# Optimization experiments

Hardware: AMD Instinct MI355X
Metric: run time of the kernel (lower is better)

Reference implementation:

```python
import jax, jax.numpy as jnp
import numpy as np

HEADS = 6
G = 4  # redundant group repeat factor in the original module
EPS = 1e-5


def _dw_bn(x, w, gamma, beta, mean, var):
    # depthwise 3x3 conv (stride 1, pad 1, no bias) + BatchNorm (eval mode)
    C = x.shape[1]
    y = jax.lax.conv_general_dilated(
        x, w, window_strides=(1, 1), padding=[(1, 1), (1, 1)],
        dimension_numbers=('NCHW', 'OIHW', 'NCHW'), feature_group_count=C)
    inv = gamma / jnp.sqrt(var + EPS)
    return y * inv[None, :, None, None] + (beta - mean * inv)[None, :, None, None]


def setup_inputs() -> dict:
    key = jax.random.key(0)
    ks = jax.random.split(key, 20)
    B, Cin, Cout, H, W = 8, 192, 192, 28, 28
    inp = {
        'x': jax.random.normal(ks[0], (B, H * W, Cin), jnp.float32),
        'h': H, 'w': W,
    }
    s = 0.1
    for i, p in enumerate(['q', 'k', 'v']):
        inp[f'dw{p}_w'] = jax.random.normal(ks[1 + i], (Cin, 1, 3, 3), jnp.float32) * s
        bk = jax.random.split(ks[4 + i], 4)
        inp[f'bn{p}_g'] = 1.0 + 0.1 * jax.random.normal(bk[0], (Cin,), jnp.float32)
        inp[f'bn{p}_b'] = 0.1 * jax.random.normal(bk[1], (Cin,), jnp.float32)
        inp[f'bn{p}_m'] = 0.1 * jax.random.normal(bk[2], (Cin,), jnp.float32)
        inp[f'bn{p}_v'] = jax.random.uniform(bk[3], (Cin,), jnp.float32, 0.5, 1.5)
        inp[f'p{p}_w'] = jax.random.normal(ks[7 + i], (Cout, Cin), jnp.float32) * (Cin ** -0.5)
        inp[f'p{p}_b'] = 0.01 * jax.random.normal(ks[10 + i], (Cout,), jnp.float32)
    inp['po_w'] = jax.random.normal(ks[13], (Cout, Cout), jnp.float32) * (Cout ** -0.5)
    inp['po_b'] = 0.01 * jax.random.normal(ks[14], (Cout,), jnp.float32)
    return inp


def reference(x, h, w,
              dwq_w, bnq_g, bnq_b, bnq_m, bnq_v, pq_w, pq_b,
              dwk_w, bnk_g, bnk_b, bnk_m, bnk_v, pk_w, pk_b,
              dwv_w, bnv_g, bnv_b, bnv_m, bnv_v, pv_w, pv_b,
              po_w, po_b):
    B, N, Cin = x.shape
    Cout = pq_w.shape[0]
    ch = Cout // HEADS  # per-head channel dim
    x4 = jnp.transpose(x, (0, 2, 1)).reshape(B, Cin, h, w)

    q = _dw_bn(x4, dwq_w, bnq_g, bnq_b, bnq_m, bnq_v)
    k = _dw_bn(x4, dwk_w, bnk_g, bnk_b, bnk_m, bnk_v)
    v = _dw_bn(x4, dwv_w, bnv_g, bnv_b, bnv_m, bnv_v)

    # 1x1 conv projections
    q = jnp.einsum('oc,bcij->boij', pq_w, q) + pq_b[None, :, None, None]
    k = jnp.einsum('oc,bcij->boij', pk_w, k) + pk_b[None, :, None, None]
    v = jnp.einsum('oc,bcij->boij', pv_w, v) + pv_b[None, :, None, None]

    # split heads: channels are (head, ch) ordered -> (B, heads, ch, h, w)
    qh = q.reshape(B, HEADS, ch, h, w)
    kh = k.reshape(B, HEADS, ch, h, w)
    vh = v.reshape(B, HEADS, ch, h, w)

    scale = Cout ** -0.5  # NOTE: original scales by dim_out**-0.5, not head_dim
    score = jnp.einsum('bhcij,bhckl->bhijkl', qh, kh) * scale
    attn = jax.nn.softmax(score.reshape(B, HEADS, h, w, h * w), axis=-1)
    attn = attn.reshape(B, HEADS, h, w, h, w)

    out = jnp.einsum('bhijkl,bhckl->bhcij', attn, vh)  # (B, heads, ch, h, w)
    # original output channel order is (ch, heads) via 'b c h g i j -> b (c h) g i j'
    out = jnp.transpose(out, (0, 2, 1, 3, 4))  # (B, ch, heads, h, w)
    out = jnp.broadcast_to(out[:, :, :, None], (B, ch, HEADS, G, h, w))
    out = out.reshape(B, ch * HEADS, G, h, w)

    y = jnp.einsum('oc,bcgij->bogij', po_w, out) + po_b[None, :, None, None, None]
    return y
```

## Files before the change

kernel.cpp:

```cpp
#include <hip/hip_runtime.h>
#include <math.h>

namespace {
constexpr int kB = 8;
constexpr int kC = 192;
constexpr int kH = 28;
constexpr int kW = 28;
constexpr int kN = 784;
constexpr int kHEADS = 6;
constexpr int kG = 4;
constexpr float kEPS = 1e-5f;
constexpr float kSCALE = 0.07216878364870322f;
constexpr int kNP = 800;
constexpr int kXP = 832;

constexpr int kDWB = kB * 196;
constexpr int kWCV = 192;
constexpr int kKVP = 32;
constexpr int kXAP = 192;
}

typedef __attribute__((ext_vector_type(8))) short bf16x8;
typedef __attribute__((ext_vector_type(4))) float f32x4;

static __device__ __forceinline__ unsigned short f2bf(float f) {
    union { float f; unsigned int u; } v; v.f = f;
    unsigned int r = v.u + 0x7fffu + ((v.u >> 16) & 1u);
    return (unsigned short)(r >> 16);
}

__global__ __launch_bounds__(192) void dwprep_kernel(
    const float* __restrict__ x,
    const float* __restrict__ wq, const float* __restrict__ gq,
    const float* __restrict__ bq, const float* __restrict__ mq,
    const float* __restrict__ vq,
    const float* __restrict__ wk, const float* __restrict__ gk,
    const float* __restrict__ bk, const float* __restrict__ mk,
    const float* __restrict__ vk,
    const float* __restrict__ wv, const float* __restrict__ gv,
    const float* __restrict__ bv, const float* __restrict__ mv,
    const float* __restrict__ vv,
    const float* __restrict__ pqw, const float* __restrict__ pkw,
    const float* __restrict__ pvw, const float* __restrict__ pow_,
    unsigned short* __restrict__ xq, unsigned short* __restrict__ xk,
    unsigned short* __restrict__ xv,
    unsigned short* __restrict__ Wq, unsigned short* __restrict__ Wk,
    unsigned short* __restrict__ Wv, unsigned short* __restrict__ Wo,
    unsigned short* __restrict__ Kb, unsigned short* __restrict__ Vb)
{
    const int bx = blockIdx.x;
    const int t = threadIdx.x;

    if (bx < kDWB) {
        const int c = t;
        const int b = bx / 196;
        const int p0 = (bx % 196) * 4;

        float wwq[9], wwk[9], wwv[9];
#pragma unroll
        for (int i = 0; i < 9; ++i) {
            wwq[i] = wq[c * 9 + i];
            wwk[i] = wk[c * 9 + i];
            wwv[i] = wv[c * 9 + i];
        }
        const float invq = gq[c] * rsqrtf(vq[c] + kEPS);
        const float addq = bq[c] - mq[c] * invq;
        const float invk = gk[c] * rsqrtf(vk[c] + kEPS);
        const float addk = bk[c] - mk[c] * invk;
        const float invv = gv[c] * rsqrtf(vv[c] + kEPS);
        const float addv = bv[c] - mv[c] * invv;

        const float* xb = x + (size_t)b * kN * kC + c;
#pragma unroll
        for (int p = 0; p < 4; ++p) {
            const int n = p0 + p;
            const int i = n / kW;
            const int j = n % kW;
            float aq = 0.f, ak = 0.f, av = 0.f;
#pragma unroll
            for (int di = -1; di <= 1; ++di) {
                const int ii = i + di;
                if (ii < 0 || ii >= kH) continue;
#pragma unroll
                for (int dj = -1; dj <= 1; ++dj) {
                    const int jj = j + dj;
                    if (jj < 0 || jj >= kW) continue;
                    const float xvl = xb[(size_t)(ii * kW + jj) * kC];
                    const int tap = (di + 1) * 3 + (dj + 1);
                    aq += xvl * wwq[tap];
                    ak += xvl * wwk[tap];
                    av += xvl * wwv[tap];
                }
            }
            const size_t o = ((size_t)b * kXP + n) * kC + c;
            xq[o] = f2bf(aq * invq + addq);
            xk[o] = f2bf(ak * invk + addk);
            xv[o] = f2bf(av * invv + addv);
        }
    } else if (bx < kDWB + kWCV) {
        const int qidx = (bx - kDWB) * 192 + t;
        const int e0 = qidx * 4;
        const int mat = e0 / (kC * kC);
        const int r = e0 % (kC * kC);
        if (mat < 3) {
            const float* src = (mat == 0) ? pqw : (mat == 1) ? pkw : pvw;
            unsigned short* dst = (mat == 0) ? Wq : (mat == 1) ? Wk : Wv;
            const f32x4 v = *(const f32x4*)&src[r];
            ushort4 p;
            p.x = f2bf(v[0]); p.y = f2bf(v[1]); p.z = f2bf(v[2]); p.w = f2bf(v[3]);
            *(ushort4*)&dst[r] = p;
        } else {
            const int o = r / kC, c0 = r % kC;
            ushort4 p;
            unsigned short* pp = &p.x;
#pragma unroll
            for (int e = 0; e < 4; ++e) {
                const int c = c0 + e;
                pp[e] = f2bf(pow_[o * kC + (c & 31) * kHEADS + (c >> 5)]);
            }
            *(ushort4*)&Wo[o * kC + c0] = p;
        }
    } else if (bx < kDWB + kWCV + kKVP) {
        const int idx8 = (bx - kDWB - kWCV) * 192 + t;
        const ushort4 z = {0, 0, 0, 0};
        if (idx8 < 3072) {
            const int bh = idx8 / 64, k = idx8 % 64;
            unsigned short* p = Kb + (size_t)bh * kNP * 32 + kN * 32 + k * 8;
            *(ushort4*)p = z; *(ushort4*)(p + 4) = z;
        } else {
            const int c2 = idx8 - 3072;
            const int bh = c2 / 64, rem = c2 % 64;
            const int ch = rem >> 1, half = rem & 1;
            unsigned short* p = Vb + ((size_t)bh * 32 + ch) * kNP + kN + half * 8;
            *(ushort4*)p = z; *(ushort4*)(p + 4) = z;
        }
    } else {
        const int c = (bx - kDWB - kWCV - kKVP) * 192 + t;
        const int arr = c / 9216;
        const int r = c % 9216;
        const int b = r / 1152, rem = r % 1152;
        const int row = kN + rem / 24;
        const int col8 = (rem % 24) * 8;
        const size_t XSZ = (size_t)kB * kXP * kC;
        unsigned short* p = xq + (size_t)arr * XSZ + ((size_t)b * kXP + row) * kC + col8;
        const ushort4 z = {0, 0, 0, 0};
        *(ushort4*)p = z; *(ushort4*)(p + 4) = z;
    }
}

__global__ __launch_bounds__(256) void proj_kernel(
    const unsigned short* __restrict__ Xq, const unsigned short* __restrict__ Xk,
    const unsigned short* __restrict__ Xv,
    const unsigned short* __restrict__ Wq, const unsigned short* __restrict__ Wk,
    const unsigned short* __restrict__ Wv,
    const float* __restrict__ bq, const float* __restrict__ bk,
    const float* __restrict__ bv,
    unsigned short* __restrict__ Qb, unsigned short* __restrict__ Kb,
    unsigned short* __restrict__ Vb)
{
    const int br = blockIdx.z % 3;
    const int b  = blockIdx.z / 3;
    const unsigned short* X = (br == 0) ? Xq : (br == 1) ? Xk : Xv;
    const unsigned short* W = (br == 0) ? Wq : (br == 1) ? Wk : Wv;
    const float* bias       = (br == 0) ? bq : (br == 1) ? bk : bv;

    const int n0 = blockIdx.x * 64, o0 = blockIdx.y * 64;
    const int t = threadIdx.x, l = t & 63, w = t >> 6;
    const int q16 = l & 15, u = l >> 4;
    const int ob = o0 + (w >> 1) * 32;
    const int nb = n0 + (w & 1) * 32;

    f32x4 a00 = {0,0,0,0}, a01 = {0,0,0,0}, a10 = {0,0,0,0}, a11 = {0,0,0,0};
    const unsigned short* Wr0 = W + (size_t)(ob + q16) * kC + u * 8;
    const unsigned short* Wr1 = W + (size_t)(ob + 16 + q16) * kC + u * 8;
    const unsigned short* Xr0 = X + ((size_t)b * kXP + nb + q16) * kC + u * 8;
    const unsigned short* Xr1 = X + ((size_t)b * kXP + nb + 16 + q16) * kC + u * 8;
#pragma unroll
    for (int kk = 0; kk < 6; ++kk) {
        const bf16x8 wa0 = *(const bf16x8*)(Wr0 + kk * 32);
        const bf16x8 wa1 = *(const bf16x8*)(Wr1 + kk * 32);
        const bf16x8 xa0 = *(const bf16x8*)(Xr0 + kk * 32);
        const bf16x8 xa1 = *(const bf16x8*)(Xr1 + kk * 32);
        a00 = __builtin_amdgcn_mfma_f32_16x16x32_bf16(wa0, xa0, a00, 0, 0, 0);
        a01 = __builtin_amdgcn_mfma_f32_16x16x32_bf16(wa0, xa1, a01, 0, 0, 0);
        a10 = __builtin_amdgcn_mfma_f32_16x16x32_bf16(wa1, xa0, a10, 0, 0, 0);
        a11 = __builtin_amdgcn_mfma_f32_16x16x32_bf16(wa1, xa1, a11, 0, 0, 0);
    }

    const float sc = (br == 0) ? kSCALE : 1.0f;
#pragma unroll
    for (int ot = 0; ot < 2; ++ot) {
        const int obase = ob + ot * 16;
        const int hh = obase >> 5;
        const int chb = (obase & 31) + 4 * u;
        const f32x4 bi = *(const f32x4*)&bias[obase + 4 * u];
#pragma unroll
        for (int nt = 0; nt < 2; ++nt) {
            const f32x4 A = (ot == 0) ? (nt == 0 ? a00 : a01)
                                      : (nt == 0 ? a10 : a11);
            const int n = nb + nt * 16 + q16;
            if (n >= kNP) continue;
            if (br < 2) {
                ushort4 p;
                p.x = f2bf((A[0] + bi[0]) * sc);
                p.y = f2bf((A[1] + bi[1]) * sc);
                p.z = f2bf((A[2] + bi[2]) * sc);
                p.w = f2bf((A[3] + bi[3]) * sc);
                unsigned short* dst = ((br == 0) ? Qb : Kb) +
                    ((size_t)(b * kHEADS + hh) * kNP + n) * 32 + chb;
                *(ushort4*)dst = p;
            } else {
                unsigned short* dst = Vb +
                    ((size_t)(b * kHEADS + hh) * 32 + chb) * kNP + n;
                dst[0 * kNP] = f2bf(A[0] + bi[0]);
                dst[1 * kNP] = f2bf(A[1] + bi[1]);
                dst[2 * kNP] = f2bf(A[2] + bi[2]);
                dst[3 * kNP] = f2bf(A[3] + bi[3]);
            }
        }
    }
}

__global__ __launch_bounds__(256) void attn_kernel(
    const unsigned short* __restrict__ Qbf, const unsigned short* __restrict__ Kbf,
    const unsigned short* __restrict__ Vbf, unsigned short* __restrict__ AO)
{
    const int wid = blockIdx.x * 4 + (threadIdx.x >> 6);
    const int l = threadIdx.x & 63;
    const int qt = wid % 49;
    const int h  = (wid / 49) % kHEADS;
    const int b  = wid / (49 * kHEADS);
    const int i0 = qt * 16;
    const int q16 = l & 15;
    const int u = l >> 4;

    const unsigned short* Qp = Qbf + ((size_t)(b * kHEADS + h) * kNP + i0) * 32;
    const unsigned short* Kp = Kbf + (size_t)(b * kHEADS + h) * kNP * 32;
    const unsigned short* Vr0 = Vbf + ((size_t)(b * kHEADS + h) * 32 + q16) * kNP;
    const unsigned short* Vr1 = Vr0 + (size_t)16 * kNP;

    const bf16x8 qa = *(const bf16x8*)(Qp + q16 * 32 + u * 8);

    f32x4 oa0 = {0.f, 0.f, 0.f, 0.f};
    f32x4 oa1 = {0.f, 0.f, 0.f, 0.f};
    float m = -1e30f, lsum = 0.f;

    for (int tile = 0; tile < 25; ++tile) {
        const int t0 = tile * 32;
        const bf16x8 ka0 = *(const bf16x8*)(Kp + (size_t)(t0 + q16) * 32 + u * 8);
        const bf16x8 ka1 = *(const bf16x8*)(Kp + (size_t)(t0 + 16 + q16) * 32 + u * 8);
        f32x4 d0 = {0.f, 0.f, 0.f, 0.f};
        f32x4 d1 = {0.f, 0.f, 0.f, 0.f};
        d0 = __builtin_amdgcn_mfma_f32_16x16x32_bf16(ka0, qa, d0, 0, 0, 0);
        d1 = __builtin_amdgcn_mfma_f32_16x16x32_bf16(ka1, qa, d1, 0, 0, 0);
        if (t0 + 16 >= kN) {
            d1[0] = -1e30f; d1[1] = -1e30f; d1[2] = -1e30f; d1[3] = -1e30f;
        }
        float tm = fmaxf(fmaxf(fmaxf(d0[0], d0[1]), fmaxf(d0[2], d0[3])),
                         fmaxf(fmaxf(d1[0], d1[1]), fmaxf(d1[2], d1[3])));
        tm = fmaxf(tm, __shfl_xor(tm, 16));
        tm = fmaxf(tm, __shfl_xor(tm, 32));
        if (!__all(tm <= m + 8.0f)) {
            const float newm = fmaxf(m, tm);
            const float alpha = __expf(m - newm);
            m = newm;
            lsum *= alpha;
            const float al0 = __shfl(alpha, u * 4 + 0);
            const float al1 = __shfl(alpha, u * 4 + 1);
            const float al2 = __shfl(alpha, u * 4 + 2);
            const float al3 = __shfl(alpha, u * 4 + 3);
            oa0[0] *= al0; oa0[1] *= al1; oa0[2] *= al2; oa0[3] *= al3;
            oa1[0] *= al0; oa1[1] *= al1; oa1[2] *= al2; oa1[3] *= al3;
        }
        const float e0 = __expf(d0[0] - m), e1 = __expf(d0[1] - m);
        const float e2 = __expf(d0[2] - m), e3 = __expf(d0[3] - m);
        const float e4 = __expf(d1[0] - m), e5 = __expf(d1[1] - m);
        const float e6 = __expf(d1[2] - m), e7 = __expf(d1[3] - m);
        lsum += (((e0 + e1) + (e2 + e3)) + ((e4 + e5) + (e6 + e7)));
        union { unsigned int w[4]; bf16x8 v; } pa;
        asm("v_cvt_pk_bf16_f32 %0, %1, %2" : "=v"(pa.w[0]) : "v"(e0), "v"(e1));
        asm("v_cvt_pk_bf16_f32 %0, %1, %2" : "=v"(pa.w[1]) : "v"(e2), "v"(e3));
        asm("v_cvt_pk_bf16_f32 %0, %1, %2" : "=v"(pa.w[2]) : "v"(e4), "v"(e5));
        asm("v_cvt_pk_bf16_f32 %0, %1, %2" : "=v"(pa.w[3]) : "v"(e6), "v"(e7));
        union { ushort4 hlf[2]; bf16x8 v; } v0, v1;
        v0.hlf[0] = *(const ushort4*)(Vr0 + t0 + 4 * u);
        v0.hlf[1] = *(const ushort4*)(Vr0 + t0 + 16 + 4 * u);
        v1.hlf[0] = *(const ushort4*)(Vr1 + t0 + 4 * u);
        v1.hlf[1] = *(const ushort4*)(Vr1 + t0 + 16 + 4 * u);
        oa0 = __builtin_amdgcn_mfma_f32_16x16x32_bf16(pa.v, v0.v, oa0, 0, 0, 0);
        oa1 = __builtin_amdgcn_mfma_f32_16x16x32_bf16(pa.v, v1.v, oa1, 0, 0, 0);
    }
    lsum += __shfl_xor(lsum, 16);
    lsum += __shfl_xor(lsum, 32);
    const float rinv = 1.0f / lsum;
    const float r0 = __shfl(rinv, u * 4 + 0);
    const float r1 = __shfl(rinv, u * 4 + 1);
    const float r2 = __shfl(rinv, u * 4 + 2);
    const float r3 = __shfl(rinv, u * 4 + 3);
    unsigned short* aw = AO + ((size_t)b * kXP + i0 + 4 * u) * kC + h * 32 + q16;
    aw[0 * kC + 0]  = f2bf(oa0[0] * r0);
    aw[1 * kC + 0]  = f2bf(oa0[1] * r1);
    aw[2 * kC + 0]  = f2bf(oa0[2] * r2);
    aw[3 * kC + 0]  = f2bf(oa0[3] * r3);
    aw[0 * kC + 16] = f2bf(oa1[0] * r0);
    aw[1 * kC + 16] = f2bf(oa1[1] * r1);
    aw[2 * kC + 16] = f2bf(oa1[2] * r2);
    aw[3 * kC + 16] = f2bf(oa1[3] * r3);
}

__global__ __launch_bounds__(256) void outproj_kernel(
    const unsigned short* __restrict__ AO, const unsigned short* __restrict__ Wo,
    const float* __restrict__ pob, float* __restrict__ Y)
{
    __shared__ float outs[64][68];

    const int b = blockIdx.z;
    const int n0 = blockIdx.x * 64, o0 = blockIdx.y * 64;
    const int t = threadIdx.x, l = t & 63, w = t >> 6;
    const int q16 = l & 15, u = l >> 4;
    const int ob = o0 + w * 16;

    f32x4 c0 = {0,0,0,0}, c1 = {0,0,0,0}, c2 = {0,0,0,0}, c3 = {0,0,0,0};
    const unsigned short* Wr = Wo + (size_t)(ob + q16) * kC + u * 8;
    const unsigned short* Ar = AO + ((size_t)b * kXP + n0 + q16) * kC + u * 8;
#pragma unroll
    for (int kk = 0; kk < 6; ++kk) {
        const bf16x8 a = *(const bf16x8*)(Wr + kk * 32);
        const bf16x8 x0 = *(const bf16x8*)(Ar + (size_t)0 * 16 * kC + kk * 32);
        const bf16x8 x1 = *(const bf16x8*)(Ar + (size_t)1 * 16 * kC + kk * 32);
        const bf16x8 x2 = *(const bf16x8*)(Ar + (size_t)2 * 16 * kC + kk * 32);
        const bf16x8 x3 = *(const bf16x8*)(Ar + (size_t)3 * 16 * kC + kk * 32);
        c0 = __builtin_amdgcn_mfma_f32_16x16x32_bf16(a, x0, c0, 0, 0, 0);
        c1 = __builtin_amdgcn_mfma_f32_16x16x32_bf16(a, x1, c1, 0, 0, 0);
        c2 = __builtin_amdgcn_mfma_f32_16x16x32_bf16(a, x2, c2, 0, 0, 0);
        c3 = __builtin_amdgcn_mfma_f32_16x16x32_bf16(a, x3, c3, 0, 0, 0);
    }
    const f32x4 bi = *(const f32x4*)&pob[ob + 4 * u];
#pragma unroll
    for (int nt = 0; nt < 4; ++nt) {
        const f32x4 A = (nt == 0) ? c0 : (nt == 1) ? c1 : (nt == 2) ? c2 : c3;
#pragma unroll
        for (int r = 0; r < 4; ++r)
            outs[w * 16 + 4 * u + r][nt * 16 + q16] = A[r] + bi[r];
    }
    __syncthreads();

    const int ol = t >> 2;
    const int nq = (t & 3) * 16;
    const int nbase = n0 + nq;
    if (nbase < kN) {
        f32x4 v0 = *(const f32x4*)&outs[ol][nq + 0];
        f32x4 v1 = *(const f32x4*)&outs[ol][nq + 4];
        f32x4 v2 = *(const f32x4*)&outs[ol][nq + 8];
        f32x4 v3 = *(const f32x4*)&outs[ol][nq + 12];
        const int o = o0 + ol;
        float* yp = Y + (((size_t)b * kC + o) * kG) * kN + nbase;
#pragma unroll
        for (int g = 0; g < kG; ++g) {
            *(f32x4*)&yp[g * kN + 0]  = v0;
            *(f32x4*)&yp[g * kN + 4]  = v1;
            *(f32x4*)&yp[g * kN + 8]  = v2;
            *(f32x4*)&yp[g * kN + 12] = v3;
        }
    }
}

extern "C" void kernel_launch(void* const* d_in, const int* in_sizes, int n_in,
                              void* d_out, int out_size, void* d_ws, size_t ws_size,
                              hipStream_t stream) {
    const float* x     = (const float*)d_in[0];
    const float* dwq_w = (const float*)d_in[3];
    const float* bnq_g = (const float*)d_in[4];
    const float* bnq_b = (const float*)d_in[5];
    const float* bnq_m = (const float*)d_in[6];
    const float* bnq_v = (const float*)d_in[7];
    const float* pq_w  = (const float*)d_in[8];
    const float* pq_b  = (const float*)d_in[9];
    const float* dwk_w = (const float*)d_in[10];
    const float* bnk_g = (const float*)d_in[11];
    const float* bnk_b = (const float*)d_in[12];
    const float* bnk_m = (const float*)d_in[13];
    const float* bnk_v = (const float*)d_in[14];
    const float* pk_w  = (const float*)d_in[15];
    const float* pk_b  = (const float*)d_in[16];
    const float* dwv_w = (const float*)d_in[17];
    const float* bnv_g = (const float*)d_in[18];
    const float* bnv_b = (const float*)d_in[19];
    const float* bnv_m = (const float*)d_in[20];
    const float* bnv_v = (const float*)d_in[21];
    const float* pv_w  = (const float*)d_in[22];
    const float* pv_b  = (const float*)d_in[23];
    const float* po_w  = (const float*)d_in[24];
    const float* po_b  = (const float*)d_in[25];

    unsigned short* ws = (unsigned short*)d_ws;
    const size_t XSZ = (size_t)kB * kXP * kC;
    const size_t QSZ = (size_t)kB * kHEADS * kNP * 32;
    unsigned short* Xq = ws;
    unsigned short* Xk = Xq + XSZ;
    unsigned short* Xv = Xk + XSZ;
    unsigned short* AO = Xv + XSZ;
    unsigned short* Qb = AO + XSZ;
    unsigned short* Kb = Qb + QSZ;
    unsigned short* Vb = Kb + QSZ;
    unsigned short* Wq = Vb + QSZ;
    unsigned short* Wk = Wq + kC * kC;
    unsigned short* Wv = Wk + kC * kC;
    unsigned short* Wo = Wv + kC * kC;

    dwprep_kernel<<<dim3(kDWB + kWCV + kKVP + kXAP), dim3(192), 0, stream>>>(
        x,
        dwq_w, bnq_g, bnq_b, bnq_m, bnq_v,
        dwk_w, bnk_g, bnk_b, bnk_m, bnk_v,
        dwv_w, bnv_g, bnv_b, bnv_m, bnv_v,
        pq_w, pk_w, pv_w, po_w,
        Xq, Xk, Xv, Wq, Wk, Wv, Wo, Kb, Vb);

    proj_kernel<<<dim3(13, 3, kB * 3), dim3(256), 0, stream>>>(
        Xq, Xk, Xv, Wq, Wk, Wv, pq_b, pk_b, pv_b, Qb, Kb, Vb);

    attn_kernel<<<dim3(kB * kHEADS * 49 / 4), dim3(256), 0, stream>>>(
        Qb, Kb, Vb, AO);

    outproj_kernel<<<dim3(13, 3, kB), dim3(256), 0, stream>>>(
        AO, Wo, po_b, (float*)d_out);
}
```

Before: 79.15 us.

## Fuse depthwise conv into projection and attention into output projection

The depthwise conv+BN now writes its bf16 result into shared memory, and the same block runs the QKV 1x1 projection MFMAs on it, so the Xq/Xk/Xv intermediates never go through global memory. The attention kernel now handles all six heads of a 16-query tile per block, keeps the head outputs in LDS, and applies the output projection in place, which removes the AO buffer and one launch. Weight conversion and padding zeroing move to a small separate prep kernel. The cost is fewer, larger blocks (392 blocks of 384 threads) and narrower output stores (scalar instead of f32x4), which may hurt write coalescing for the large output.

```diff
diff --git a/kernel.cpp b/kernel.cpp
--- a/kernel.cpp
+++ b/kernel.cpp
@@ -12,12 +12,6 @@
 constexpr float kEPS = 1e-5f;
 constexpr float kSCALE = 0.07216878364870322f;
 constexpr int kNP = 800;
-constexpr int kXP = 832;
-
-constexpr int kDWB = kB * 196;
-constexpr int kWCV = 192;
-constexpr int kKVP = 32;
-constexpr int kXAP = 192;
 }
 
 typedef __attribute__((ext_vector_type(8))) short bf16x8;
@@ -29,77 +23,16 @@
     return (unsigned short)(r >> 16);
 }
 
-__global__ __launch_bounds__(192) void dwprep_kernel(
-    const float* __restrict__ x,
-    const float* __restrict__ wq, const float* __restrict__ gq,
-    const float* __restrict__ bq, const float* __restrict__ mq,
-    const float* __restrict__ vq,
-    const float* __restrict__ wk, const float* __restrict__ gk,
-    const float* __restrict__ bk, const float* __restrict__ mk,
-    const float* __restrict__ vk,
-    const float* __restrict__ wv, const float* __restrict__ gv,
-    const float* __restrict__ bv, const float* __restrict__ mv,
-    const float* __restrict__ vv,
+__global__ __launch_bounds__(256) void prep_kernel(
     const float* __restrict__ pqw, const float* __restrict__ pkw,
     const float* __restrict__ pvw, const float* __restrict__ pow_,
-    unsigned short* __restrict__ xq, unsigned short* __restrict__ xk,
-    unsigned short* __restrict__ xv,
     unsigned short* __restrict__ Wq, unsigned short* __restrict__ Wk,
     unsigned short* __restrict__ Wv, unsigned short* __restrict__ Wo,
     unsigned short* __restrict__ Kb, unsigned short* __restrict__ Vb)
 {
-    const int bx = blockIdx.x;
-    const int t = threadIdx.x;
-
-    if (bx < kDWB) {
-        const int c = t;
-        const int b = bx / 196;
-        const int p0 = (bx % 196) * 4;
-
-        float wwq[9], wwk[9], wwv[9];
-#pragma unroll
-        for (int i = 0; i < 9; ++i) {
-            wwq[i] = wq[c * 9 + i];
-            wwk[i] = wk[c * 9 + i];
-            wwv[i] = wv[c * 9 + i];
-        }
-        const float invq = gq[c] * rsqrtf(vq[c] + kEPS);
-        const float addq = bq[c] - mq[c] * invq;
-        const float invk = gk[c] * rsqrtf(vk[c] + kEPS);
-        const float addk = bk[c] - mk[c] * invk;
-        const float invv = gv[c] * rsqrtf(vv[c] + kEPS);
-        const float addv = bv[c] - mv[c] * invv;
-
-        const float* xb = x + (size_t)b * kN * kC + c;
-#pragma unroll
-        for (int p = 0; p < 4; ++p) {
-            const int n = p0 + p;
-            const int i = n / kW;
-            const int j = n % kW;
-            float aq = 0.f, ak = 0.f, av = 0.f;
-#pragma unroll
-            for (int di = -1; di <= 1; ++di) {
-                const int ii = i + di;
-                if (ii < 0 || ii >= kH) continue;
-#pragma unroll
-                for (int dj = -1; dj <= 1; ++dj) {
-                    const int jj = j + dj;
-                    if (jj < 0 || jj >= kW) continue;
-                    const float xvl = xb[(size_t)(ii * kW + jj) * kC];
-                    const int tap = (di + 1) * 3 + (dj + 1);
-                    aq += xvl * wwq[tap];
-                    ak += xvl * wwk[tap];
-                    av += xvl * wwv[tap];
-                }
-            }
-            const size_t o = ((size_t)b * kXP + n) * kC + c;
-            xq[o] = f2bf(aq * invq + addq);
-            xk[o] = f2bf(ak * invk + addk);
-            xv[o] = f2bf(av * invv + addv);
-        }
-    } else if (bx < kDWB + kWCV) {
-        const int qidx = (bx - kDWB) * 192 + t;
-        const int e0 = qidx * 4;
+    const int aux = blockIdx.x * 256 + threadIdx.x;
+    if (aux < 36864) {
+        const int e0 = aux * 4;
         const int mat = e0 / (kC * kC);
         const int r = e0 % (kC * kC);
         if (mat < 3) {
@@ -120,8 +53,8 @@
             }
             *(ushort4*)&Wo[o * kC + c0] = p;
         }
-    } else if (bx < kDWB + kWCV + kKVP) {
-        const int idx8 = (bx - kDWB - kWCV) * 192 + t;
+    } else {
+        const int idx8 = aux - 36864;
         const ushort4 z = {0, 0, 0, 0};
         if (idx8 < 3072) {
             const int bh = idx8 / 64, k = idx8 % 64;
@@ -134,233 +67,232 @@
             unsigned short* p = Vb + ((size_t)bh * 32 + ch) * kNP + kN + half * 8;
             *(ushort4*)p = z; *(ushort4*)(p + 4) = z;
         }
-    } else {
-        const int c = (bx - kDWB - kWCV - kKVP) * 192 + t;
-        const int arr = c / 9216;
-        const int r = c % 9216;
-        const int b = r / 1152, rem = r % 1152;
-        const int row = kN + rem / 24;
-        const int col8 = (rem % 24) * 8;
-        const size_t XSZ = (size_t)kB * kXP * kC;
-        unsigned short* p = xq + (size_t)arr * XSZ + ((size_t)b * kXP + row) * kC + col8;
-        const ushort4 z = {0, 0, 0, 0};
-        *(ushort4*)p = z; *(ushort4*)(p + 4) = z;
-    }
-}
-
-__global__ __launch_bounds__(256) void proj_kernel(
-    const unsigned short* __restrict__ Xq, const unsigned short* __restrict__ Xk,
-    const unsigned short* __restrict__ Xv,
+    }
+}
+
+__global__ __launch_bounds__(384) void dwproj_kernel(
+    const float* __restrict__ x,
+    const float* __restrict__ wq, const float* __restrict__ gq,
+    const float* __restrict__ bq, const float* __restrict__ mq,
+    const float* __restrict__ vq,
+    const float* __restrict__ wk, const float* __restrict__ gk,
+    const float* __restrict__ bk, const float* __restrict__ mk,
+    const float* __restrict__ vk,
+    const float* __restrict__ wv, const float* __restrict__ gv,
+    const float* __restrict__ bv, const float* __restrict__ mv,
+    const float* __restrict__ vv,
     const unsigned short* __restrict__ Wq, const unsigned short* __restrict__ Wk,
     const unsigned short* __restrict__ Wv,
-    const float* __restrict__ bq, const float* __restrict__ bk,
-    const float* __restrict__ bv,
+    const float* __restrict__ pqb, const float* __restrict__ pkb,
+    const float* __restrict__ pvb,
     unsigned short* __restrict__ Qb, unsigned short* __restrict__ Kb,
     unsigned short* __restrict__ Vb)
 {
-    const int br = blockIdx.z % 3;
-    const int b  = blockIdx.z / 3;
-    const unsigned short* X = (br == 0) ? Xq : (br == 1) ? Xk : Xv;
-    const unsigned short* W = (br == 0) ? Wq : (br == 1) ? Wk : Wv;
-    const float* bias       = (br == 0) ? bq : (br == 1) ? bk : bv;
-
-    const int n0 = blockIdx.x * 64, o0 = blockIdx.y * 64;
-    const int t = threadIdx.x, l = t & 63, w = t >> 6;
-    const int q16 = l & 15, u = l >> 4;
-    const int ob = o0 + (w >> 1) * 32;
-    const int nb = n0 + (w & 1) * 32;
-
-    f32x4 a00 = {0,0,0,0}, a01 = {0,0,0,0}, a10 = {0,0,0,0}, a11 = {0,0,0,0};
-    const unsigned short* Wr0 = W + (size_t)(ob + q16) * kC + u * 8;
-    const unsigned short* Wr1 = W + (size_t)(ob + 16 + q16) * kC + u * 8;
-    const unsigned short* Xr0 = X + ((size_t)b * kXP + nb + q16) * kC + u * 8;
-    const unsigned short* Xr1 = X + ((size_t)b * kXP + nb + 16 + q16) * kC + u * 8;
-#pragma unroll
-    for (int kk = 0; kk < 6; ++kk) {
-        const bf16x8 wa0 = *(const bf16x8*)(Wr0 + kk * 32);
-        const bf16x8 wa1 = *(const bf16x8*)(Wr1 + kk * 32);
-        const bf16x8 xa0 = *(const bf16x8*)(Xr0 + kk * 32);
-        const bf16x8 xa1 = *(const bf16x8*)(Xr1 + kk * 32);
-        a00 = __builtin_amdgcn_mfma_f32_16x16x32_bf16(wa0, xa0, a00, 0, 0, 0);
-        a01 = __builtin_amdgcn_mfma_f32_16x16x32_bf16(wa0, xa1, a01, 0, 0, 0);
-        a10 = __builtin_amdgcn_mfma_f32_16x16x32_bf16(wa1, xa0, a10, 0, 0, 0);
-        a11 = __builtin_amdgcn_mfma_f32_16x16x32_bf16(wa1, xa1, a11, 0, 0, 0);
-    }
-
-    const float sc = (br == 0) ? kSCALE : 1.0f;
-#pragma unroll
-    for (int ot = 0; ot < 2; ++ot) {
-        const int obase = ob + ot * 16;
-        const int hh = obase >> 5;
-        const int chb = (obase & 31) + 4 * u;
-        const f32x4 bi = *(const f32x4*)&bias[obase + 4 * u];
-#pragma unroll
-        for (int nt = 0; nt < 2; ++nt) {
-            const f32x4 A = (ot == 0) ? (nt == 0 ? a00 : a01)
-                                      : (nt == 0 ? a10 : a11);
-            const int n = nb + nt * 16 + q16;
-            if (n >= kNP) continue;
-            if (br < 2) {
-                ushort4 p;
-                p.x = f2bf((A[0] + bi[0]) * sc);
-                p.y = f2bf((A[1] + bi[1]) * sc);
-                p.z = f2bf((A[2] + bi[2]) * sc);
-                p.w = f2bf((A[3] + bi[3]) * sc);
-                unsigned short* dst = ((br == 0) ? Qb : Kb) +
-                    ((size_t)(b * kHEADS + hh) * kNP + n) * 32 + chb;
-                *(ushort4*)dst = p;
-            } else {
-                unsigned short* dst = Vb +
-                    ((size_t)(b * kHEADS + hh) * 32 + chb) * kNP + n;
-                dst[0 * kNP] = f2bf(A[0] + bi[0]);
-                dst[1 * kNP] = f2bf(A[1] + bi[1]);
-                dst[2 * kNP] = f2bf(A[2] + bi[2]);
-                dst[3 * kNP] = f2bf(A[3] + bi[3]);
+    __shared__ unsigned short Xs[3][16][200];
+
+    const int b  = blockIdx.x / 49;
+    const int n0 = (blockIdx.x % 49) * 16;
+    const int t = threadIdx.x;
+
+    {
+        const int c  = t % 192;
+        const int ph = t / 192;
+        float wwq[9], wwk[9], wwv[9];
+#pragma unroll
+        for (int i = 0; i < 9; ++i) {
+            wwq[i] = wq[c * 9 + i];
+            wwk[i] = wk[c * 9 + i];
+            wwv[i] = wv[c * 9 + i];
+        }
+        const float invq = gq[c] * rsqrtf(vq[c] + kEPS);
+        const float addq = bq[c] - mq[c] * invq;
+        const float invk = gk[c] * rsqrtf(vk[c] + kEPS);
+        const float addk = bk[c] - mk[c] * invk;
+        const float invv = gv[c] * rsqrtf(vv[c] + kEPS);
+        const float addv = bv[c] - mv[c] * invv;
+        const float* xb = x + (size_t)b * kN * kC + c;
+#pragma unroll
+        for (int p = 0; p < 8; ++p) {
+            const int pos = ph * 8 + p;
+            const int n = n0 + pos;
+            const int i = n / kW, j = n % kW;
+            float aq = 0.f, ak = 0.f, av = 0.f;
+#pragma unroll
+            for (int di = -1; di <= 1; ++di) {
+                const int ii = i + di;
+                if (ii < 0 || ii >= kH) continue;
+#pragma unroll
+                for (int dj = -1; dj <= 1; ++dj) {
+                    const int jj = j + dj;
+                    if (jj < 0 || jj >= kW) continue;
+                    const float xvl = xb[(size_t)(ii * kW + jj) * kC];
+                    const int tap = (di + 1) * 3 + (dj + 1);
+                    aq += xvl * wwq[tap];
+                    ak += xvl * wwk[tap];
+                    av += xvl * wwv[tap];
+                }
             }
-        }
-    }
-}
-
-__global__ __launch_bounds__(256) void attn_kernel(
+            Xs[0][pos][c] = f2bf(aq * invq + addq);
+            Xs[1][pos][c] = f2bf(ak * invk + addk);
+            Xs[2][pos][c] = f2bf(av * invv + addv);
+        }
+    }
+    __syncthreads();
+
+    const int w = t >> 6, l = t & 63, q16 = l & 15, u = l >> 4;
+#pragma unroll
+    for (int k6 = 0; k6 < 6; ++k6) {
+        const int unit = w * 6 + k6;
+        const int br = unit / 12;
+        const int ob = (unit % 12) * 16;
+        const unsigned short* W = (br == 0) ? Wq : (br == 1) ? Wk : Wv;
+        const float* bias       = (br == 0) ? pqb : (br == 1) ? pkb : pvb;
+
+        f32x4 acc = {0.f, 0.f, 0.f, 0.f};
+        const unsigned short* Wr = W + (size_t)(ob + q16) * kC + u * 8;
+#pragma unroll
+        for (int kk = 0; kk < 6; ++kk) {
+            const bf16x8 wa = *(const bf16x8*)(Wr + kk * 32);
+            const bf16x8 xa = *(const bf16x8*)&Xs[br][q16][u * 8 + kk * 32];
+            acc = __builtin_amdgcn_mfma_f32_16x16x32_bf16(wa, xa, acc, 0, 0, 0);
+        }
+        const int hh = ob >> 5;
+        const int ch0 = (ob & 31) + 4 * u;
+        const f32x4 bi = *(const f32x4*)&bias[ob + 4 * u];
+        const int n = n0 + q16;
+        if (br < 2) {
+            const float sc = (br == 0) ? kSCALE : 1.0f;
+            ushort4 p;
+            p.x = f2bf((acc[0] + bi[0]) * sc);
+            p.y = f2bf((acc[1] + bi[1]) * sc);
+            p.z = f2bf((acc[2] + bi[2]) * sc);
+            p.w = f2bf((acc[3] + bi[3]) * sc);
+            unsigned short* dst = ((br == 0) ? Qb : Kb) +
+                ((size_t)(b * kHEADS + hh) * kNP + n) * 32 + ch0;
+            *(ushort4*)dst = p;
+        } else {
+            unsigned short* dst = Vb +
+                ((size_t)(b * kHEADS + hh) * 32 + ch0) * kNP + n;
+            dst[0 * kNP] = f2bf(acc[0] + bi[0]);
+            dst[1 * kNP] = f2bf(acc[1] + bi[1]);
+            dst[2 * kNP] = f2bf(acc[2] + bi[2]);
+            dst[3 * kNP] = f2bf(acc[3] + bi[3]);
+        }
+    }
+}
+
+__global__ __launch_bounds__(384) void attnout_kernel(
     const unsigned short* __restrict__ Qbf, const unsigned short* __restrict__ Kbf,
-    const unsigned short* __restrict__ Vbf, unsigned short* __restrict__ AO)
+    const unsigned short* __restrict__ Vbf, const unsigned short* __restrict__ Wo,
+    const float* __restrict__ pob, float* __restrict__ Y)
 {
-    const int wid = blockIdx.x * 4 + (threadIdx.x >> 6);
-    const int l = threadIdx.x & 63;
-    const int qt = wid % 49;
-    const int h  = (wid / 49) % kHEADS;
-    const int b  = wid / (49 * kHEADS);
-    const int i0 = qt * 16;
+    __shared__ unsigned short AOs[16][200];
+
+    const int b  = blockIdx.x / 49;
+    const int i0 = (blockIdx.x % 49) * 16;
+    const int t = threadIdx.x;
+    const int h = t >> 6;
+    const int l = t & 63;
     const int q16 = l & 15;
     const int u = l >> 4;
 
-    const unsigned short* Qp = Qbf + ((size_t)(b * kHEADS + h) * kNP + i0) * 32;
-    const unsigned short* Kp = Kbf + (size_t)(b * kHEADS + h) * kNP * 32;
-    const unsigned short* Vr0 = Vbf + ((size_t)(b * kHEADS + h) * 32 + q16) * kNP;
-    const unsigned short* Vr1 = Vr0 + (size_t)16 * kNP;
-
-    const bf16x8 qa = *(const bf16x8*)(Qp + q16 * 32 + u * 8);
-
-    f32x4 oa0 = {0.f, 0.f, 0.f, 0.f};
-    f32x4 oa1 = {0.f, 0.f, 0.f, 0.f};
-    float m = -1e30f, lsum = 0.f;
-
-    for (int tile = 0; tile < 25; ++tile) {
-        const int t0 = tile * 32;
-        const bf16x8 ka0 = *(const bf16x8*)(Kp + (size_t)(t0 + q16) * 32 + u * 8);
-        const bf16x8 ka1 = *(const bf16x8*)(Kp + (size_t)(t0 + 16 + q16) * 32 + u * 8);
-        f32x4 d0 = {0.f, 0.f, 0.f, 0.f};
-        f32x4 d1 = {0.f, 0.f, 0.f, 0.f};
-        d0 = __builtin_amdgcn_mfma_f32_16x16x32_bf16(ka0, qa, d0, 0, 0, 0);
-        d1 = __builtin_amdgcn_mfma_f32_16x16x32_bf16(ka1, qa, d1, 0, 0, 0);
-        if (t0 + 16 >= kN) {
-            d1[0] = -1e30f; d1[1] = -1e30f; d1[2] = -1e30f; d1[3] = -1e30f;
-        }
-        float tm = fmaxf(fmaxf(fmaxf(d0[0], d0[1]), fmaxf(d0[2], d0[3])),
-                         fmaxf(fmaxf(d1[0], d1[1]), fmaxf(d1[2], d1[3])));
-        tm = fmaxf(tm, __shfl_xor(tm, 16));
-        tm = fmaxf(tm, __shfl_xor(tm, 32));
-        if (!__all(tm <= m + 8.0f)) {
-            const float newm = fmaxf(m, tm);
-            const float alpha = __expf(m - newm);
-            m = newm;
-            lsum *= alpha;
-            const float al0 = __shfl(alpha, u * 4 + 0);
-            const float al1 = __shfl(alpha, u * 4 + 1);
-            const float al2 = __shfl(alpha, u * 4 + 2);
-            const float al3 = __shfl(alpha, u * 4 + 3);
-            oa0[0] *= al0; oa0[1] *= al1; oa0[2] *= al2; oa0[3] *= al3;
-            oa1[0] *= al0; oa1[1] *= al1; oa1[2] *= al2; oa1[3] *= al3;
-        }
-        const float e0 = __expf(d0[0] - m), e1 = __expf(d0[1] - m);
-        const float e2 = __expf(d0[2] - m), e3 = __expf(d0[3] - m);
-        const float e4 = __expf(d1[0] - m), e5 = __expf(d1[1] - m);
-        const float e6 = __expf(d1[2] - m), e7 = __expf(d1[3] - m);
-        lsum += (((e0 + e1) + (e2 + e3)) + ((e4 + e5) + (e6 + e7)));
-        union { unsigned int w[4]; bf16x8 v; } pa;
-        asm("v_cvt_pk_bf16_f32 %0, %1, %2" : "=v"(pa.w[0]) : "v"(e0), "v"(e1));
-        asm("v_cvt_pk_bf16_f32 %0, %1, %2" : "=v"(pa.w[1]) : "v"(e2), "v"(e3));
-        asm("v_cvt_pk_bf16_f32 %0, %1, %2" : "=v"(pa.w[2]) : "v"(e4), "v"(e5));
-        asm("v_cvt_pk_bf16_f32 %0, %1, %2" : "=v"(pa.w[3]) : "v"(e6), "v"(e7));
-        union { ushort4 hlf[2]; bf16x8 v; } v0, v1;
-        v0.hlf[0] = *(const ushort4*)(Vr0 + t0 + 4 * u);
-        v0.hlf[1] = *(const ushort4*)(Vr0 + t0 + 16 + 4 * u);
-        v1.hlf[0] = *(const ushort4*)(Vr1 + t0 + 4 * u);
-        v1.hlf[1] = *(const ushort4*)(Vr1 + t0 + 16 + 4 * u);
-        oa0 = __builtin_amdgcn_mfma_f32_16x16x32_bf16(pa.v, v0.v, oa0, 0, 0, 0);
-        oa1 = __builtin_amdgcn_mfma_f32_16x16x32_bf16(pa.v, v1.v, oa1, 0, 0, 0);
-    }
-    lsum += __shfl_xor(lsum, 16);
-    lsum += __shfl_xor(lsum, 32);
-    const float rinv = 1.0f / lsum;
-    const float r0 = __shfl(rinv, u * 4 + 0);
-    const float r1 = __shfl(rinv, u * 4 + 1);
-    const float r2 = __shfl(rinv, u * 4 + 2);
-    const float r3 = __shfl(rinv, u * 4 + 3);
-    unsigned short* aw = AO + ((size_t)b * kXP + i0 + 4 * u) * kC + h * 32 + q16;
-    aw[0 * kC + 0]  = f2bf(oa0[0] * r0);
-    aw[1 * kC + 0]  = f2bf(oa0[1] * r1);
-    aw[2 * kC + 0]  = f2bf(oa0[2] * r2);
-    aw[3 * kC + 0]  = f2bf(oa0[3] * r3);
-    aw[0 * kC + 16] = f2bf(oa1[0] * r0);
-    aw[1 * kC + 16] = f2bf(oa1[1] * r1);
-    aw[2 * kC + 16] = f2bf(oa1[2] * r2);
-    aw[3 * kC + 16] = f2bf(oa1[3] * r3);
-}
-
-__global__ __launch_bounds__(256) void outproj_kernel(
-    const unsigned short* __restrict__ AO, const unsigned short* __restrict__ Wo,
-    const float* __restrict__ pob, float* __restrict__ Y)
-{
-    __shared__ float outs[64][68];
-
-    const int b = blockIdx.z;
-    const int n0 = blockIdx.x * 64, o0 = blockIdx.y * 64;
-    const int t = threadIdx.x, l = t & 63, w = t >> 6;
-    const int q16 = l & 15, u = l >> 4;
-    const int ob = o0 + w * 16;
-
-    f32x4 c0 = {0,0,0,0}, c1 = {0,0,0,0}, c2 = {0,0,0,0}, c3 = {0,0,0,0};
-    const unsigned short* Wr = Wo + (size_t)(ob + q16) * kC + u * 8;
-    const unsigned short* Ar = AO + ((size_t)b * kXP + n0 + q16) * kC + u * 8;
-#pragma unroll
-    for (int kk = 0; kk < 6; ++kk) {
-        const bf16x8 a = *(const bf16x8*)(Wr + kk * 32);
-        const bf16x8 x0 = *(const bf16x8*)(Ar + (size_t)0 * 16 * kC + kk * 32);
-        const bf16x8 x1 = *(const bf16x8*)(Ar + (size_t)1 * 16 * kC + kk * 32);
-        const bf16x8 x2 = *(const bf16x8*)(Ar + (size_t)2 * 16 * kC + kk * 32);
-        const bf16x8 x3 = *(const bf16x8*)(Ar + (size_t)3 * 16 * kC + kk * 32);
-        c0 = __builtin_amdgcn_mfma_f32_16x16x32_bf16(a, x0, c0, 0, 0, 0);
-        c1 = __builtin_amdgcn_mfma_f32_16x16x32_bf16(a, x1, c1, 0, 0, 0);
-        c2 = __builtin_amdgcn_mfma_f32_16x16x32_bf16(a, x2, c2, 0, 0, 0);
-        c3 = __builtin_amdgcn_mfma_f32_16x16x32_bf16(a, x3, c3, 0, 0, 0);
-    }
-    const f32x4 bi = *(const f32x4*)&pob[ob + 4 * u];
-#pragma unroll
-    for (int nt = 0; nt < 4; ++nt) {
-        const f32x4 A = (nt == 0) ? c0 : (nt == 1) ? c1 : (nt == 2) ? c2 : c3;
-#pragma unroll
-        for (int r = 0; r < 4; ++r)
-            outs[w * 16 + 4 * u + r][nt * 16 + q16] = A[r] + bi[r];
+    {
+        const unsigned short* Qp = Qbf + ((size_t)(b * kHEADS + h) * kNP + i0) * 32;
+        const unsigned short* Kp = Kbf + (size_t)(b * kHEADS + h) * kNP * 32;
+        const unsigned short* Vr0 = Vbf + ((size_t)(b * kHEADS + h) * 32 + q16) * kNP;
+        const unsigned short* Vr1 = Vr0 + (size_t)16 * kNP;
+
+        const bf16x8 qa = *(const bf16x8*)(Qp + q16 * 32 + u * 8);
+
+        f32x4 oa0 = {0.f, 0.f, 0.f, 0.f};
+        f32x4 oa1 = {0.f, 0.f, 0.f, 0.f};
+        float m = -1e30f, lsum = 0.f;
+
+        for (int tile = 0; tile < 25; ++tile) {
+            const int t0 = tile * 32;
+            const bf16x8 ka0 = *(const bf16x8*)(Kp + (size_t)(t0 + q16) * 32 + u * 8);
+            const bf16x8 ka1 = *(const bf16x8*)(Kp + (size_t)(t0 + 16 + q16) * 32 + u * 8);
+            f32x4 d0 = {0.f, 0.f, 0.f, 0.f};
+            f32x4 d1 = {0.f, 0.f, 0.f, 0.f};
+            d0 = __builtin_amdgcn_mfma_f32_16x16x32_bf16(ka0, qa, d0, 0, 0, 0);
+            d1 = __builtin_amdgcn_mfma_f32_16x16x32_bf16(ka1, qa, d1, 0, 0, 0);
+            if (t0 + 16 >= kN) {
+                d1[0] = -1e30f; d1[1] = -1e30f; d1[2] = -1e30f; d1[3] = -1e30f;
+            }
+            float tm = fmaxf(fmaxf(fmaxf(d0[0], d0[1]), fmaxf(d0[2], d0[3])),
+                             fmaxf(fmaxf(d1[0], d1[1]), fmaxf(d1[2], d1[3])));
+            tm = fmaxf(tm, __shfl_xor(tm, 16));
+            tm = fmaxf(tm, __shfl_xor(tm, 32));
+            if (!__all(tm <= m + 8.0f)) {
+                const float newm = fmaxf(m, tm);
+                const float alpha = __expf(m - newm);
+                m = newm;
+                lsum *= alpha;
+                const float al0 = __shfl(alpha, u * 4 + 0);
+                const float al1 = __shfl(alpha, u * 4 + 1);
+                const float al2 = __shfl(alpha, u * 4 + 2);
+                const float al3 = __shfl(alpha, u * 4 + 3);
+                oa0[0] *= al0; oa0[1] *= al1; oa0[2] *= al2; oa0[3] *= al3;
+                oa1[0] *= al0; oa1[1] *= al1; oa1[2] *= al2; oa1[3] *= al3;
+            }
+            const float e0 = __expf(d0[0] - m), e1 = __expf(d0[1] - m);
+            const float e2 = __expf(d0[2] - m), e3 = __expf(d0[3] - m);
+            const float e4 = __expf(d1[0] - m), e5 = __expf(d1[1] - m);
+            const float e6 = __expf(d1[2] - m), e7 = __expf(d1[3] - m);
+            lsum += (((e0 + e1) + (e2 + e3)) + ((e4 + e5) + (e6 + e7)));
+            union { unsigned int w[4]; bf16x8 v; } pa;
+            asm("v_cvt_pk_bf16_f32 %0, %1, %2" : "=v"(pa.w[0]) : "v"(e0), "v"(e1));
+            asm("v_cvt_pk_bf16_f32 %0, %1, %2" : "=v"(pa.w[1]) : "v"(e2), "v"(e3));
+            asm("v_cvt_pk_bf16_f32 %0, %1, %2" : "=v"(pa.w[2]) : "v"(e4), "v"(e5));
+            asm("v_cvt_pk_bf16_f32 %0, %1, %2" : "=v"(pa.w[3]) : "v"(e6), "v"(e7));
+            union { ushort4 hlf[2]; bf16x8 v; } v0, v1;
+            v0.hlf[0] = *(const ushort4*)(Vr0 + t0 + 4 * u);
+            v0.hlf[1] = *(const ushort4*)(Vr0 + t0 + 16 + 4 * u);
+            v1.hlf[0] = *(const ushort4*)(Vr1 + t0 + 4 * u);
+            v1.hlf[1] = *(const ushort4*)(Vr1 + t0 + 16 + 4 * u);
+            oa0 = __builtin_amdgcn_mfma_f32_16x16x32_bf16(pa.v, v0.v, oa0, 0, 0, 0);
+            oa1 = __builtin_amdgcn_mfma_f32_16x16x32_bf16(pa.v, v1.v, oa1, 0, 0, 0);
+        }
+        lsum += __shfl_xor(lsum, 16);
+        lsum += __shfl_xor(lsum, 32);
+        const float rinv = 1.0f / lsum;
+        const float r0 = __shfl(rinv, u * 4 + 0);
+        const float r1 = __shfl(rinv, u * 4 + 1);
+        const float r2 = __shfl(rinv, u * 4 + 2);
+        const float r3 = __shfl(rinv, u * 4 + 3);
+        AOs[4 * u + 0][h * 32 + q16] = f2bf(oa0[0] * r0);
+        AOs[4 * u + 1][h * 32 + q16] = f2bf(oa0[1] * r1);
+        AOs[4 * u + 2][h * 32 + q16] = f2bf(oa0[2] * r2);
+        AOs[4 * u + 3][h * 32 + q16] = f2bf(oa0[3] * r3);
+        AOs[4 * u + 0][h * 32 + 16 + q16] = f2bf(oa1[0] * r0);
+        AOs[4 * u + 1][h * 32 + 16 + q16] = f2bf(oa1[1] * r1);
+        AOs[4 * u + 2][h * 32 + 16 + q16] = f2bf(oa1[2] * r2);
+        AOs[4 * u + 3][h * 32 + 16 + q16] = f2bf(oa1[3] * r3);
     }
     __syncthreads();
 
-    const int ol = t >> 2;
-    const int nq = (t & 3) * 16;
-    const int nbase = n0 + nq;
-    if (nbase < kN) {
-        f32x4 v0 = *(const f32x4*)&outs[ol][nq + 0];
-        f32x4 v1 = *(const f32x4*)&outs[ol][nq + 4];
-        f32x4 v2 = *(const f32x4*)&outs[ol][nq + 8];
-        f32x4 v3 = *(const f32x4*)&outs[ol][nq + 12];
-        const int o = o0 + ol;
-        float* yp = Y + (((size_t)b * kC + o) * kG) * kN + nbase;
-#pragma unroll
-        for (int g = 0; g < kG; ++g) {
-            *(f32x4*)&yp[g * kN + 0]  = v0;
-            *(f32x4*)&yp[g * kN + 4]  = v1;
-            *(f32x4*)&yp[g * kN + 8]  = v2;
-            *(f32x4*)&yp[g * kN + 12] = v3;
+#pragma unroll
+    for (int k2 = 0; k2 < 2; ++k2) {
+        const int ob = (h * 2 + k2) * 16;
+        f32x4 acc = {0.f, 0.f, 0.f, 0.f};
+        const unsigned short* Wr = Wo + (size_t)(ob + q16) * kC + u * 8;
+#pragma unroll
+        for (int kk = 0; kk < 6; ++kk) {
+            const bf16x8 wa = *(const bf16x8*)(Wr + kk * 32);
+            const bf16x8 xa = *(const bf16x8*)&AOs[q16][u * 8 + kk * 32];
+            acc = __builtin_amdgcn_mfma_f32_16x16x32_bf16(wa, xa, acc, 0, 0, 0);
+        }
+        const f32x4 bi = *(const f32x4*)&pob[ob + 4 * u];
+        const int n = i0 + q16;
+#pragma unroll
+        for (int r = 0; r < 4; ++r) {
+            const int o = ob + 4 * u + r;
+            const float val = acc[r] + bi[r];
+            float* yp = Y + (((size_t)b * kC + o) * kG) * kN + n;
+            yp[0 * kN] = val;
+            yp[1 * kN] = val;
+            yp[2 * kN] = val;
+            yp[3 * kN] = val;
         }
     }
 }
@@ -394,13 +326,8 @@
     const float* po_b  = (const float*)d_in[25];
 
     unsigned short* ws = (unsigned short*)d_ws;
-    const size_t XSZ = (size_t)kB * kXP * kC;
     const size_t QSZ = (size_t)kB * kHEADS * kNP * 32;
-    unsigned short* Xq = ws;
-    unsigned short* Xk = Xq + XSZ;
-    unsigned short* Xv = Xk + XSZ;
-    unsigned short* AO = Xv + XSZ;
-    unsigned short* Qb = AO + XSZ;
+    unsigned short* Qb = ws;
     unsigned short* Kb = Qb + QSZ;
     unsigned short* Vb = Kb + QSZ;
     unsigned short* Wq = Vb + QSZ;
@@ -408,20 +335,16 @@
     unsigned short* Wv = Wk + kC * kC;
     unsigned short* Wo = Wv + kC * kC;
 
-    dwprep_kernel<<<dim3(kDWB + kWCV + kKVP + kXAP), dim3(192), 0, stream>>>(
+    prep_kernel<<<dim3(168), dim3(256), 0, stream>>>(
+        pq_w, pk_w, pv_w, po_w, Wq, Wk, Wv, Wo, Kb, Vb);
+
+    dwproj_kernel<<<dim3(kB * 49), dim3(384), 0, stream>>>(
         x,
         dwq_w, bnq_g, bnq_b, bnq_m, bnq_v,
         dwk_w, bnk_g, bnk_b, bnk_m, bnk_v,
         dwv_w, bnv_g, bnv_b, bnv_m, bnv_v,
-        pq_w, pk_w, pv_w, po_w,
-        Xq, Xk, Xv, Wq, Wk, Wv, Wo, Kb, Vb);
-
-    proj_kernel<<<dim3(13, 3, kB * 3), dim3(256), 0, stream>>>(
-        Xq, Xk, Xv, Wq, Wk, Wv, pq_b, pk_b, pv_b, Qb, Kb, Vb);
-
-    attn_kernel<<<dim3(kB * kHEADS * 49 / 4), dim3(256), 0, stream>>>(
-        Qb, Kb, Vb, AO);
-
-    outproj_kernel<<<dim3(13, 3, kB), dim3(256), 0, stream>>>(
-        AO, Wo, po_b, (float*)d_out);
-}
+        Wq, Wk, Wv, pq_b, pk_b, pv_b, Qb, Kb, Vb);
+
+    attnout_kernel<<<dim3(kB * 49), dim3(384), 0, stream>>>(
+        Qb, Kb, Vb, Wo, po_b, (float*)d_out);
+}
```

Result: no change. 77.70 us (-1.8%).
